# Performance work log

Measured on AMD Instinct MI355X. Metric: run time of the kernel, lower is better.

## Reference

```python
import jax, jax.numpy as jnp
import numpy as np

EPS = 1e-5

def _bn(x, gamma, beta):
    # training-mode BatchNorm1d over (batch, points) per channel; x: [B, C, N]
    mean = x.mean(axis=(0, 2), keepdims=True)
    var = x.var(axis=(0, 2), keepdims=True)
    return gamma[None, :, None] * (x - mean) * jax.lax.rsqrt(var + EPS) + beta[None, :, None]

def _conv_nn(x, idx, W, b):
    # x: [B, Cin, N_in]; idx: [N_out, k]; W: [Cout, Cin, k]
    g = x[:, :, idx]  # gather -> [B, Cin, N_out, k]
    return jnp.einsum('bink,oik->bon', g, W) + b[None, :, None]

def setup_inputs() -> dict:
    key = jax.random.key(0)
    ks = jax.random.split(key, 8)
    B, Cin, Cout = 32, 32, 64
    Nin, Nout, K, KP = 32768, 8192, 9, 4
    s = 0.05
    return {
        'x': jax.random.normal(ks[0], (B, Cin, Nin), jnp.float32),
        'W1': jax.random.normal(ks[1], (Cout, Cin, K), jnp.float32) * s,
        'b1': jnp.zeros((Cout,), jnp.float32),
        'W2': jax.random.normal(ks[2], (Cout, Cout, K), jnp.float32) * s,
        'b2': jnp.zeros((Cout,), jnp.float32),
        'We': jax.random.normal(ks[3], (Cout, Cin), jnp.float32) * s,
        'be': jnp.zeros((Cout,), jnp.float32),
        'g1': jnp.ones((Cout,), jnp.float32), 'beta1': jnp.zeros((Cout,), jnp.float32),
        'g2': jnp.ones((Cout,), jnp.float32), 'beta2': jnp.zeros((Cout,), jnp.float32),
        'g3': jnp.ones((Cout,), jnp.float32), 'beta3': jnp.zeros((Cout,), jnp.float32),
        'idx1': jax.random.randint(ks[4], (Nout, K), 0, Nin, jnp.int32),
        'idx2': jax.random.randint(ks[5], (Nout, K), 0, Nout, jnp.int32),
        'pool_idx': jax.random.randint(ks[6], (Nout, KP), 0, Nin, jnp.int32),
    }

def reference(x, W1, b1, W2, b2, We, be, g1, beta1, g2, beta2, g3, beta3, idx1, idx2, pool_idx):
    # main branch: ConvNN -> BN -> ReLU -> ConvNN -> BN
    out = jax.nn.relu(_bn(_conv_nn(x, idx1, W1, b1), g1, beta1))
    out = _bn(_conv_nn(out, idx2, W2, b2), g2, beta2)
    # shortcut: AvgPoolNN (k=4) -> 1x1 conv expand -> BN
    pooled = x[:, :, pool_idx].mean(axis=-1)  # [B, Cin, N_out]
    identity = _bn(jnp.einsum('bin,oi->bon', pooled, We) + be[None, :, None], g3, beta3)
    return jax.nn.relu(out + identity)
```

## Files before the change

kernel.cpp:

```cpp
#include <hip/hip_runtime.h>
#include <hip/hip_bf16.h>

typedef __attribute__((ext_vector_type(8))) short short8_t;
typedef __attribute__((ext_vector_type(4))) float f32x4_t;

#define NOUT 8192
#define NIN 32768
#define MTOT 262144.0f
#define ST_STRIPES 64

#define MF(a,b,c) __builtin_amdgcn_mfma_f32_16x16x32_bf16((a),(b),(c),0,0,0)

static __device__ __forceinline__ float bf2f(ushort u) {
    union { float f; unsigned int i; } x; x.i = ((unsigned int)u) << 16; return x.f;
}
static __device__ __forceinline__ ushort f2bfx(float f) {
    union { __hip_bfloat16 h; ushort u; } v;
    v.h = __float2bfloat16(f);
    return v.u;
}
static __device__ __forceinline__ short8_t i4s8(int4 v) {
    union { int4 i; short8_t s; } u; u.i = v; return u.s;
}

static __device__ __forceinline__ short8_t bn8(int4 v, const float* a8, const float* c8) {
    ushort* pv = (ushort*)&v;
    #pragma unroll
    for (int e = 0; e < 8; ++e)
        pv[e] = f2bfx(fmaxf(a8[e] * bf2f(pv[e]) + c8[e], 0.f));
    return i4s8(v);
}

__global__ __launch_bounds__(256) void transpose_x_kernel(
    const float* __restrict__ x, ushort* __restrict__ xt)
{
    __shared__ ushort T[64][66];
    const int tid = threadIdx.x;
    const int n0 = blockIdx.x * 64, c0 = blockIdx.y * 64;
    const int lane64 = tid & 63, rb = (tid >> 6) * 16;
    #pragma unroll
    for (int r = 0; r < 16; ++r) {
        int c_l = rb + r;
        T[c_l][lane64] = f2bfx(x[(size_t)(c0 + c_l) * NIN + n0 + lane64]);
    }
    __syncthreads();
    #pragma unroll
    for (int r = 0; r < 16; ++r) {
        int n_l = rb + r;
        xt[(size_t)(n0 + n_l) * 1024 + c0 + lane64] = T[lane64][n_l];
    }
}

__global__ __launch_bounds__(256) void prep_w_kernel(
    const float* __restrict__ W1, const float* __restrict__ W2,
    const float* __restrict__ We,
    ushort* __restrict__ w1p, ushort* __restrict__ w2p, ushort* __restrict__ wep,
    float* __restrict__ stz)
{
    int t = blockIdx.x * 256 + threadIdx.x;
    const int N1 = 18432, N2 = 36864, N3 = 2048;
    if (t < 3 * ST_STRIPES * 128) stz[t] = 0.f;
    if (t < N1) {
        int e = t & 7, o = (t >> 3) & 63, seg = t >> 9;
        int fcg = seg & 3, k = seg >> 2;
        int i = fcg * 8 + e;
        w1p[t] = f2bfx(W1[o * 288 + i * 9 + k]);
    } else if (t < N1 + N2) {
        int t2 = t - N1;
        int e = t2 & 7, o = (t2 >> 3) & 63, seg = t2 >> 9;
        int fcg = seg & 3, kk = (seg >> 2) & 1, k = seg >> 3;
        int ci = kk * 32 + fcg * 8 + e;
        w2p[t2] = f2bfx(W2[o * 576 + ci * 9 + k]);
    } else if (t < N1 + N2 + N3) {
        int t3 = t - N1 - N2;
        wep[t3] = f2bfx(We[t3]);
    }
}

__global__ __launch_bounds__(512, 2) void conv1i_kernel(
    const ushort* __restrict__ xt, const int* __restrict__ idx1,
    const int* __restrict__ pool_idx, const ushort* __restrict__ w1p,
    const ushort* __restrict__ wep,
    ushort* __restrict__ out1, ushort* __restrict__ identt,
    float* __restrict__ st1g, float* __restrict__ st3g)
{
    __shared__ __align__(16) ushort Wl[18432];
    __shared__ float Ls1[128], Ls3[128];
    const int tid = threadIdx.x;
    const int lane = tid & 63, wv = tid >> 6;
    const int n = __builtin_amdgcn_readfirstlane(blockIdx.x * 8 + wv);
    const int l15 = lane & 15, fcg = lane >> 4, fc = fcg * 8;

    for (int i = tid; i < 2304; i += 512)
        ((int4*)Wl)[i] = ((const int4*)w1p)[i];
    if (tid < 128) { Ls1[tid] = 0.f; Ls3[tid] = 0.f; }

    int rows[9], prow[4];
    {
        const int* idxn = idx1 + n * 9;
        #pragma unroll
        for (int t = 0; t < 9; ++t) rows[t] = idxn[t];
        const int* pn = pool_idx + n * 4;
        #pragma unroll
        for (int t = 0; t < 4; ++t) prow[t] = pn[t];
    }
    __syncthreads();

    f32x4_t acc[2][4];
    #pragma unroll
    for (int m = 0; m < 2; ++m)
        #pragma unroll
        for (int nt = 0; nt < 4; ++nt) acc[m][nt] = (f32x4_t){0.f, 0.f, 0.f, 0.f};

    int4 A0[2], A1[2], A2[2], A3[2];

#define C1_PRE(K, A) { \
    const ushort* rp = xt + (size_t)rows[K] * 1024 + l15 * 32 + fc; \
    A[0] = *(const int4*)rp; \
    A[1] = *(const int4*)(rp + 512); }

#define C1_PPRE(KP, A) { \
    const ushort* rp = xt + (size_t)prow[KP] * 1024 + l15 * 32 + fc; \
    A[0] = *(const int4*)rp; \
    A[1] = *(const int4*)(rp + 512); }

#define C1_BODY(K, A) { \
    const ushort* wp = Wl + ((K) * 4 + fcg) * 512; \
    short8_t b0 = *(const short8_t*)(wp + l15 * 8); \
    short8_t b1 = *(const short8_t*)(wp + (16 + l15) * 8); \
    short8_t b2 = *(const short8_t*)(wp + (32 + l15) * 8); \
    short8_t b3 = *(const short8_t*)(wp + (48 + l15) * 8); \
    short8_t af0 = i4s8(A[0]), af1 = i4s8(A[1]); \
    acc[0][0] = MF(af0, b0, acc[0][0]); acc[1][0] = MF(af1, b0, acc[1][0]); \
    acc[0][1] = MF(af0, b1, acc[0][1]); acc[1][1] = MF(af1, b1, acc[1][1]); \
    acc[0][2] = MF(af0, b2, acc[0][2]); acc[1][2] = MF(af1, b2, acc[1][2]); \
    acc[0][3] = MF(af0, b3, acc[0][3]); acc[1][3] = MF(af1, b3, acc[1][3]); }

    C1_PRE(0, A0); C1_PRE(1, A1); C1_PRE(2, A2); C1_PRE(3, A3);
    C1_BODY(0, A0); C1_PRE(4, A0);
    C1_BODY(1, A1); C1_PRE(5, A1);
    C1_BODY(2, A2); C1_PRE(6, A2);
    C1_BODY(3, A3); C1_PRE(7, A3);
    C1_BODY(4, A0); C1_PRE(8, A0);
    C1_BODY(5, A1); C1_PPRE(0, A1);
    C1_BODY(6, A2); C1_PPRE(1, A2);
    C1_BODY(7, A3); C1_PPRE(2, A3);
    C1_BODY(8, A0);
#undef C1_PRE
#undef C1_BODY

    const size_t outbase = (size_t)n * 2048;
    #pragma unroll
    for (int m = 0; m < 2; ++m)
        #pragma unroll
        for (int nt = 0; nt < 4; ++nt)
            #pragma unroll
            for (int j = 0; j < 4; ++j) {
                int b = m * 16 + (lane >> 4) * 4 + j;
                int o = nt * 16 + l15;
                out1[outbase + b * 64 + o] = f2bfx(acc[m][nt][j]);
            }
    #pragma unroll
    for (int nt = 0; nt < 4; ++nt) {
        float s = 0.f, q = 0.f;
        #pragma unroll
        for (int m = 0; m < 2; ++m)
            #pragma unroll
            for (int j = 0; j < 4; ++j) { float v = acc[m][nt][j]; s += v; q += v * v; }
        s += __shfl_xor(s, 16); s += __shfl_xor(s, 32);
        q += __shfl_xor(q, 16); q += __shfl_xor(q, 32);
        if (lane < 16) {
            atomicAdd(&Ls1[nt * 16 + lane], s);
            atomicAdd(&Ls1[64 + nt * 16 + lane], q);
        }
    }

    int4 P3[2];
    C1_PPRE(3, P3);
#undef C1_PPRE
    float s0[8], s1[8];
    #pragma unroll
    for (int e = 0; e < 8; ++e) { s0[e] = 0.f; s1[e] = 0.f; }
    {
        const ushort* p;
        p = (const ushort*)&A1[0];
        #pragma unroll
        for (int e = 0; e < 8; ++e) s0[e] += bf2f(p[e]);
        p = (const ushort*)&A1[1];
        #pragma unroll
        for (int e = 0; e < 8; ++e) s1[e] += bf2f(p[e]);
        p = (const ushort*)&A2[0];
        #pragma unroll
        for (int e = 0; e < 8; ++e) s0[e] += bf2f(p[e]);
        p = (const ushort*)&A2[1];
        #pragma unroll
        for (int e = 0; e < 8; ++e) s1[e] += bf2f(p[e]);
        p = (const ushort*)&A3[0];
        #pragma unroll
        for (int e = 0; e < 8; ++e) s0[e] += bf2f(p[e]);
        p = (const ushort*)&A3[1];
        #pragma unroll
        for (int e = 0; e < 8; ++e) s1[e] += bf2f(p[e]);
        p = (const ushort*)&P3[0];
        #pragma unroll
        for (int e = 0; e < 8; ++e) s0[e] += bf2f(p[e]);
        p = (const ushort*)&P3[1];
        #pragma unroll
        for (int e = 0; e < 8; ++e) s1[e] += bf2f(p[e]);
    }
    short8_t paf0, paf1;
    {
        int4 v0, v1; ushort* p0 = (ushort*)&v0; ushort* p1 = (ushort*)&v1;
        #pragma unroll
        for (int e = 0; e < 8; ++e) {
            p0[e] = f2bfx(s0[e] * 0.25f);
            p1[e] = f2bfx(s1[e] * 0.25f);
        }
        paf0 = i4s8(v0); paf1 = i4s8(v1);
    }
    short8_t bfr[4];
    {
        const ushort* wpf = wep + l15 * 32 + fc;
        #pragma unroll
        for (int nt = 0; nt < 4; ++nt)
            bfr[nt] = *(const short8_t*)(wpf + nt * 512);
    }
    #pragma unroll
    for (int nt = 0; nt < 4; ++nt) {
        acc[0][nt] = (f32x4_t){0.f, 0.f, 0.f, 0.f};
        acc[1][nt] = (f32x4_t){0.f, 0.f, 0.f, 0.f};
        acc[0][nt] = MF(paf0, bfr[nt], acc[0][nt]);
        acc[1][nt] = MF(paf1, bfr[nt], acc[1][nt]);
    }
    #pragma unroll
    for (int m = 0; m < 2; ++m)
        #pragma unroll
        for (int nt = 0; nt < 4; ++nt)
            #pragma unroll
            for (int j = 0; j < 4; ++j) {
                int b = m * 16 + (lane >> 4) * 4 + j;
                int o = nt * 16 + l15;
                identt[outbase + b * 64 + o] = f2bfx(acc[m][nt][j]);
            }
    #pragma unroll
    for (int nt = 0; nt < 4; ++nt) {
        float s = 0.f, q = 0.f;
        #pragma unroll
        for (int m = 0; m < 2; ++m)
            #pragma unroll
            for (int j = 0; j < 4; ++j) { float v = acc[m][nt][j]; s += v; q += v * v; }
        s += __shfl_xor(s, 16); s += __shfl_xor(s, 32);
        q += __shfl_xor(q, 16); q += __shfl_xor(q, 32);
        if (lane < 16) {
            atomicAdd(&Ls3[nt * 16 + lane], s);
            atomicAdd(&Ls3[64 + nt * 16 + lane], q);
        }
    }
    __syncthreads();
    if (tid < 128) {
        atomicAdd(&st1g[(blockIdx.x & (ST_STRIPES - 1)) * 128 + tid], Ls1[tid]);
        atomicAdd(&st3g[(blockIdx.x & (ST_STRIPES - 1)) * 128 + tid], Ls3[tid]);
    }
}

__global__ __launch_bounds__(512, 2) void conv2_kernel(
    const ushort* __restrict__ out1raw, const int* __restrict__ idx2,
    const ushort* __restrict__ w2p, const float* __restrict__ ac1,
    ushort* __restrict__ out2, float* __restrict__ st)
{
    __shared__ __align__(16) ushort Wl[36864];
    __shared__ float Ls[128];
    const int tid = threadIdx.x;
    const int lane = tid & 63, wv = tid >> 6;
    const int n = __builtin_amdgcn_readfirstlane(blockIdx.x * 8 + wv);
    const int l15 = lane & 15, fcg = lane >> 4, fc = fcg * 8;

    for (int i = tid; i < 4608; i += 512)
        ((int4*)Wl)[i] = ((const int4*)w2p)[i];
    if (tid < 128) Ls[tid] = 0.f;

    int rows[9];
    {
        const int* idxn = idx2 + n * 9;
        #pragma unroll
        for (int t = 0; t < 9; ++t) rows[t] = idxn[t];
    }
    float a0r[8], c0r[8], a1r[8], c1r[8];
    #pragma unroll
    for (int e = 0; e < 8; ++e) {
        a0r[e] = ac1[fc + e];       c0r[e] = ac1[64 + fc + e];
        a1r[e] = ac1[32 + fc + e];  c1r[e] = ac1[96 + fc + e];
    }
    __syncthreads();

    f32x4_t acc[2][4];
    #pragma unroll
    for (int m = 0; m < 2; ++m)
        #pragma unroll
        for (int nt = 0; nt < 4; ++nt) acc[m][nt] = (f32x4_t){0.f, 0.f, 0.f, 0.f};

    int4 A0[4], A1[4], A2[4];

#define C2_PRE(K, A) { \
    const ushort* rp = out1raw + (size_t)rows[K] * 2048 + l15 * 64 + fc; \
    A[0] = *(const int4*)rp; \
    A[1] = *(const int4*)(rp + 32); \
    A[2] = *(const int4*)(rp + 1024); \
    A[3] = *(const int4*)(rp + 1056); }

#define C2_BODY(K, A) { \
    const ushort* wp0 = Wl + ((K) * 8 + fcg) * 512; \
    const ushort* wp1 = wp0 + 4 * 512; \
    short8_t b00 = *(const short8_t*)(wp0 + l15 * 8); \
    short8_t b10 = *(const short8_t*)(wp0 + (16 + l15) * 8); \
    short8_t b20 = *(const short8_t*)(wp0 + (32 + l15) * 8); \
    short8_t b30 = *(const short8_t*)(wp0 + (48 + l15) * 8); \
    short8_t b01 = *(const short8_t*)(wp1 + l15 * 8); \
    short8_t b11 = *(const short8_t*)(wp1 + (16 + l15) * 8); \
    short8_t b21 = *(const short8_t*)(wp1 + (32 + l15) * 8); \
    short8_t b31 = *(const short8_t*)(wp1 + (48 + l15) * 8); \
    short8_t af00 = bn8(A[0], a0r, c0r); \
    short8_t af01 = bn8(A[1], a1r, c1r); \
    short8_t af10 = bn8(A[2], a0r, c0r); \
    short8_t af11 = bn8(A[3], a1r, c1r); \
    acc[0][0] = MF(af00, b00, acc[0][0]); acc[0][0] = MF(af01, b01, acc[0][0]); \
    acc[0][1] = MF(af00, b10, acc[0][1]); acc[0][1] = MF(af01, b11, acc[0][1]); \
    acc[0][2] = MF(af00, b20, acc[0][2]); acc[0][2] = MF(af01, b21, acc[0][2]); \
    acc[0][3] = MF(af00, b30, acc[0][3]); acc[0][3] = MF(af01, b31, acc[0][3]); \
    acc[1][0] = MF(af10, b00, acc[1][0]); acc[1][0] = MF(af11, b01, acc[1][0]); \
    acc[1][1] = MF(af10, b10, acc[1][1]); acc[1][1] = MF(af11, b11, acc[1][1]); \
    acc[1][2] = MF(af10, b20, acc[1][2]); acc[1][2] = MF(af11, b21, acc[1][2]); \
    acc[1][3] = MF(af10, b30, acc[1][3]); acc[1][3] = MF(af11, b31, acc[1][3]); }

    C2_PRE(0, A0); C2_PRE(1, A1); C2_PRE(2, A2);
    C2_BODY(0, A0); C2_PRE(3, A0);
    C2_BODY(1, A1); C2_PRE(4, A1);
    C2_BODY(2, A2); C2_PRE(5, A2);
    C2_BODY(3, A0); C2_PRE(6, A0);
    C2_BODY(4, A1); C2_PRE(7, A1);
    C2_BODY(5, A2); C2_PRE(8, A2);
    C2_BODY(6, A0);
    C2_BODY(7, A1);
    C2_BODY(8, A2);
#undef C2_PRE
#undef C2_BODY

    const size_t outbase = (size_t)n * 2048;
    #pragma unroll
    for (int m = 0; m < 2; ++m)
        #pragma unroll
        for (int nt = 0; nt < 4; ++nt)
            #pragma unroll
            for (int j = 0; j < 4; ++j) {
                int b = m * 16 + (lane >> 4) * 4 + j;
                int o = nt * 16 + l15;
                out2[outbase + b * 64 + o] = f2bfx(acc[m][nt][j]);
            }
    #pragma unroll
    for (int nt = 0; nt < 4; ++nt) {
        float s = 0.f, q = 0.f;
        #pragma unroll
        for (int m = 0; m < 2; ++m)
            #pragma unroll
            for (int j = 0; j < 4; ++j) { float v = acc[m][nt][j]; s += v; q += v * v; }
        s += __shfl_xor(s, 16); s += __shfl_xor(s, 32);
        q += __shfl_xor(q, 16); q += __shfl_xor(q, 32);
        if (lane < 16) {
            atomicAdd(&Ls[nt * 16 + lane], s);
            atomicAdd(&Ls[64 + nt * 16 + lane], q);
        }
    }
    __syncthreads();
    if (tid < 128) atomicAdd(&st[(blockIdx.x & (ST_STRIPES - 1)) * 128 + tid], Ls[tid]);
}

__global__ void finalize_kernel(const float* __restrict__ st, const float* __restrict__ g,
                                const float* __restrict__ bet, float* __restrict__ ac)
{
    int o = threadIdx.x;
    if (o >= 64) return;
    float s = 0.f, q = 0.f;
    for (int i = 0; i < ST_STRIPES; ++i) { s += st[i * 128 + o]; q += st[i * 128 + 64 + o]; }
    float mean = s * (1.0f / MTOT);
    float var  = q * (1.0f / MTOT) - mean * mean;
    float a = g[o] * rsqrtf(var + 1e-5f);
    ac[o] = a;
    ac[64 + o] = bet[o] - a * mean;
}

__global__ void finalize_dual_kernel(
    const float* __restrict__ stA, const float* __restrict__ gA, const float* __restrict__ bA,
    const float* __restrict__ stB, const float* __restrict__ gB, const float* __restrict__ bB,
    float* __restrict__ acA, float* __restrict__ acB)
{
    int o = threadIdx.x;
    if (o >= 64) return;
    const float* st = blockIdx.x ? stB : stA;
    const float* g  = blockIdx.x ? gB  : gA;
    const float* bt = blockIdx.x ? bB  : bA;
    float* ac       = blockIdx.x ? acB : acA;
    float s = 0.f, q = 0.f;
    for (int i = 0; i < ST_STRIPES; ++i) { s += st[i * 128 + o]; q += st[i * 128 + 64 + o]; }
    float mean = s * (1.0f / MTOT);
    float var  = q * (1.0f / MTOT) - mean * mean;
    float a = g[o] * rsqrtf(var + 1e-5f);
    ac[o] = a;
    ac[64 + o] = bt[o] - a * mean;
}

__global__ __launch_bounds__(256) void final_combine_kernel(
    const ushort* __restrict__ out2, const ushort* __restrict__ idt,
    const float* __restrict__ ac2, const float* __restrict__ ac3,
    float* __restrict__ dout)
{
    __shared__ float tile[64][65];
    const int tid = threadIdx.x;
    const int n0 = blockIdx.x * 64, bo0 = blockIdx.y * 64;
    const int lane64 = tid & 63, rb = (tid >> 6) * 16;
    const int o = lane64;
    const float a2 = ac2[o], c2 = ac2[64 + o], a3 = ac3[o], c3 = ac3[64 + o];
    #pragma unroll
    for (int r = 0; r < 16; ++r) {
        int n_l = rb + r;
        size_t p = (size_t)(n0 + n_l) * 2048 + bo0 + lane64;
        float v = a2 * bf2f(out2[p]) + c2 + a3 * bf2f(idt[p]) + c3;
        tile[n_l][lane64] = fmaxf(v, 0.f);
    }
    __syncthreads();
    #pragma unroll
    for (int r = 0; r < 16; ++r) {
        int bo_l = rb + r;
        dout[(size_t)(bo0 + bo_l) * NOUT + n0 + lane64] = tile[lane64][bo_l];
    }
}

extern "C" void kernel_launch(void* const* d_in, const int* in_sizes, int n_in,
                              void* d_out, int out_size, void* d_ws, size_t ws_size,
                              hipStream_t stream)
{
    const float* x     = (const float*)d_in[0];
    const float* W1    = (const float*)d_in[1];
    const float* W2    = (const float*)d_in[3];
    const float* We    = (const float*)d_in[5];
    const float* g1    = (const float*)d_in[7];
    const float* beta1 = (const float*)d_in[8];
    const float* g2    = (const float*)d_in[9];
    const float* beta2 = (const float*)d_in[10];
    const float* g3    = (const float*)d_in[11];
    const float* beta3 = (const float*)d_in[12];
    const int* idx1    = (const int*)d_in[13];
    const int* idx2    = (const int*)d_in[14];
    const int* pool_idx= (const int*)d_in[15];
    float* dout = (float*)d_out;

    char* ws = (char*)d_ws;
    const size_t off_xt   = 0;
    const size_t off_out1 = 67108864;
    const size_t off_out2 = 100663296;
    const size_t off_id   = 134217728;
    const size_t off_w1p  = 167772160;
    const size_t off_w2p  = 167809024;
    const size_t off_wep  = 167882752;
    const size_t off_st   = 167886848;
    const size_t off_ac   = 167985152;
    const size_t need     = 167986688;
    if (ws_size < need) return;

    ushort* xt   = (ushort*)(ws + off_xt);
    ushort* out1 = (ushort*)(ws + off_out1);
    ushort* out2 = (ushort*)(ws + off_out2);
    ushort* idt  = (ushort*)(ws + off_id);
    ushort* w1p  = (ushort*)(ws + off_w1p);
    ushort* w2p  = (ushort*)(ws + off_w2p);
    ushort* wep  = (ushort*)(ws + off_wep);
    float*  st1  = (float*)(ws + off_st);
    float*  st2  = st1 + 64 * 128;
    float*  st3  = st1 + 2 * 64 * 128;
    float*  ac1  = (float*)(ws + off_ac);
    float*  ac2  = ac1 + 128;
    float*  ac3  = ac1 + 256;

    prep_w_kernel<<<224, 256, 0, stream>>>(W1, W2, We, w1p, w2p, wep, st1);
    transpose_x_kernel<<<dim3(512, 16), 256, 0, stream>>>(x, xt);
    conv1i_kernel<<<1024, 512, 0, stream>>>(xt, idx1, pool_idx, w1p, wep, out1, idt, st1, st3);
    finalize_dual_kernel<<<2, 64, 0, stream>>>(st1, g1, beta1, st3, g3, beta3, ac1, ac3);
    conv2_kernel<<<1024, 512, 0, stream>>>(out1, idx2, w2p, ac1, out2, st2);
    finalize_kernel<<<1, 64, 0, stream>>>(st2, g2, beta2, ac2);
    final_combine_kernel<<<dim3(128, 32), 256, 0, stream>>>(out2, idt, ac2, ac3, dout);
}
```

Measured before the change: 174.4 us.

## Stream gathered rows into LDS via async global_load_lds double buffering

```diff
diff --git a/kernel.cpp b/kernel.cpp
--- a/kernel.cpp
+++ b/kernel.cpp
@@ -10,6 +10,8 @@
 #define ST_STRIPES 64
 
 #define MF(a,b,c) __builtin_amdgcn_mfma_f32_16x16x32_bf16((a),(b),(c),0,0,0)
+#define SB() __builtin_amdgcn_sched_barrier(0)
+#define VW(N) asm volatile("s_waitcnt vmcnt(" #N ")" ::: "memory")
 
 static __device__ __forceinline__ float bf2f(ushort u) {
     union { float f; unsigned int i; } x; x.i = ((unsigned int)u) << 16; return x.f;
@@ -22,6 +24,11 @@
 static __device__ __forceinline__ short8_t i4s8(int4 v) {
     union { int4 i; short8_t s; } u; u.i = v; return u.s;
 }
+static __device__ __forceinline__ void gll16(const ushort* g, ushort* l) {
+    __builtin_amdgcn_global_load_lds(
+        (const __attribute__((address_space(1))) void*)(g),
+        (__attribute__((address_space(3))) void*)(l), 16, 0, 0);
+}
 
 static __device__ __forceinline__ short8_t bn8(int4 v, const float* a8, const float* c8) {
     ushort* pv = (ushort*)&v;
@@ -36,18 +43,20 @@
 {
     __shared__ ushort T[64][66];
     const int tid = threadIdx.x;
-    const int n0 = blockIdx.x * 64, c0 = blockIdx.y * 64;
+    const int n0 = blockIdx.x * 64;
+    const int b0 = (blockIdx.y >> 2) * 8, g = blockIdx.y & 3;
     const int lane64 = tid & 63, rb = (tid >> 6) * 16;
     #pragma unroll
     for (int r = 0; r < 16; ++r) {
         int c_l = rb + r;
-        T[c_l][lane64] = f2bfx(x[(size_t)(c0 + c_l) * NIN + n0 + lane64]);
+        int row = (b0 + (c_l >> 3)) * 32 + g * 8 + (c_l & 7);
+        T[c_l][lane64] = f2bfx(x[(size_t)row * NIN + n0 + lane64]);
     }
     __syncthreads();
     #pragma unroll
     for (int r = 0; r < 16; ++r) {
         int n_l = rb + r;
-        xt[(size_t)(n0 + n_l) * 1024 + c0 + lane64] = T[lane64][n_l];
+        xt[(size_t)(n0 + n_l) * 1024 + g * 256 + b0 * 8 + lane64] = T[lane64][n_l];
     }
 }
 
@@ -85,11 +94,14 @@
     float* __restrict__ st1g, float* __restrict__ st3g)
 {
     __shared__ __align__(16) ushort Wl[18432];
+    __shared__ __align__(16) ushort Ar[16384];
     __shared__ float Ls1[128], Ls3[128];
     const int tid = threadIdx.x;
     const int lane = tid & 63, wv = tid >> 6;
     const int n = __builtin_amdgcn_readfirstlane(blockIdx.x * 8 + wv);
     const int l15 = lane & 15, fcg = lane >> 4, fc = fcg * 8;
+    ushort* S0 = Ar + wv * 2048;
+    ushort* S1 = S0 + 1024;
 
     for (int i = tid; i < 2304; i += 512)
         ((int4*)Wl)[i] = ((const int4*)w1p)[i];
@@ -112,41 +124,43 @@
         #pragma unroll
         for (int nt = 0; nt < 4; ++nt) acc[m][nt] = (f32x4_t){0.f, 0.f, 0.f, 0.f};
 
-    int4 A0[2], A1[2], A2[2], A3[2];
-
-#define C1_PRE(K, A) { \
-    const ushort* rp = xt + (size_t)rows[K] * 1024 + l15 * 32 + fc; \
-    A[0] = *(const int4*)rp; \
-    A[1] = *(const int4*)(rp + 512); }
-
-#define C1_PPRE(KP, A) { \
-    const ushort* rp = xt + (size_t)prow[KP] * 1024 + l15 * 32 + fc; \
-    A[0] = *(const int4*)rp; \
-    A[1] = *(const int4*)(rp + 512); }
-
-#define C1_BODY(K, A) { \
+#define C1_ISSUE(K, S) { \
+    const ushort* src = xt + (size_t)rows[K] * 1024 + lane * 8; \
+    gll16(src, (S)); \
+    gll16(src + 512, (S) + 512); }
+
+#define C1_BODY(K, S) { \
     const ushort* wp = Wl + ((K) * 4 + fcg) * 512; \
     short8_t b0 = *(const short8_t*)(wp + l15 * 8); \
     short8_t b1 = *(const short8_t*)(wp + (16 + l15) * 8); \
     short8_t b2 = *(const short8_t*)(wp + (32 + l15) * 8); \
     short8_t b3 = *(const short8_t*)(wp + (48 + l15) * 8); \
-    short8_t af0 = i4s8(A[0]), af1 = i4s8(A[1]); \
+    short8_t af0 = *(const short8_t*)((S) + fcg * 256 + l15 * 8); \
+    short8_t af1 = *(const short8_t*)((S) + fcg * 256 + 128 + l15 * 8); \
     acc[0][0] = MF(af0, b0, acc[0][0]); acc[1][0] = MF(af1, b0, acc[1][0]); \
     acc[0][1] = MF(af0, b1, acc[0][1]); acc[1][1] = MF(af1, b1, acc[1][1]); \
     acc[0][2] = MF(af0, b2, acc[0][2]); acc[1][2] = MF(af1, b2, acc[1][2]); \
     acc[0][3] = MF(af0, b3, acc[0][3]); acc[1][3] = MF(af1, b3, acc[1][3]); }
 
-    C1_PRE(0, A0); C1_PRE(1, A1); C1_PRE(2, A2); C1_PRE(3, A3);
-    C1_BODY(0, A0); C1_PRE(4, A0);
-    C1_BODY(1, A1); C1_PRE(5, A1);
-    C1_BODY(2, A2); C1_PRE(6, A2);
-    C1_BODY(3, A3); C1_PRE(7, A3);
-    C1_BODY(4, A0); C1_PRE(8, A0);
-    C1_BODY(5, A1); C1_PPRE(0, A1);
-    C1_BODY(6, A2); C1_PPRE(1, A2);
-    C1_BODY(7, A3); C1_PPRE(2, A3);
-    C1_BODY(8, A0);
-#undef C1_PRE
+    C1_ISSUE(0, S0); C1_ISSUE(1, S1); SB();
+    VW(2); SB(); C1_BODY(0, S0); SB(); C1_ISSUE(2, S0); SB();
+    VW(2); SB(); C1_BODY(1, S1); SB(); C1_ISSUE(3, S1); SB();
+    VW(2); SB(); C1_BODY(2, S0); SB(); C1_ISSUE(4, S0); SB();
+    VW(2); SB(); C1_BODY(3, S1); SB(); C1_ISSUE(5, S1); SB();
+    VW(2); SB(); C1_BODY(4, S0); SB(); C1_ISSUE(6, S0); SB();
+    VW(2); SB(); C1_BODY(5, S1); SB(); C1_ISSUE(7, S1); SB();
+    VW(2); SB(); C1_BODY(6, S0); SB(); C1_ISSUE(8, S0); SB();
+    VW(2); SB(); C1_BODY(7, S1); SB();
+    int4 Pa0, Pa1, Pb0, Pb1, Pc0, Pc1, Pd0, Pd1;
+#define C1_PLOAD(KP, X, Y) { \
+    const ushort* rp = xt + (size_t)prow[KP] * 1024 + fcg * 256 + l15 * 8; \
+    X = *(const int4*)rp; Y = *(const int4*)(rp + 128); }
+    C1_PLOAD(0, Pa0, Pa1); C1_PLOAD(1, Pb0, Pb1);
+    C1_PLOAD(2, Pc0, Pc1); C1_PLOAD(3, Pd0, Pd1);
+#undef C1_PLOAD
+    SB();
+    VW(8); SB(); C1_BODY(8, S0);
+#undef C1_ISSUE
 #undef C1_BODY
 
     const size_t outbase = (size_t)n * 2048;
@@ -158,7 +172,7 @@
             for (int j = 0; j < 4; ++j) {
                 int b = m * 16 + (lane >> 4) * 4 + j;
                 int o = nt * 16 + l15;
-                out1[outbase + b * 64 + o] = f2bfx(acc[m][nt][j]);
+                out1[outbase + (o >> 3) * 256 + b * 8 + (o & 7)] = f2bfx(acc[m][nt][j]);
             }
     #pragma unroll
     for (int nt = 0; nt < 4; ++nt) {
@@ -175,36 +189,34 @@
         }
     }
 
-    int4 P3[2];
-    C1_PPRE(3, P3);
-#undef C1_PPRE
     float s0[8], s1[8];
     #pragma unroll
     for (int e = 0; e < 8; ++e) { s0[e] = 0.f; s1[e] = 0.f; }
     {
         const ushort* p;
-        p = (const ushort*)&A1[0];
+        p = (const ushort*)&Pa0; \
+        
         #pragma unroll
         for (int e = 0; e < 8; ++e) s0[e] += bf2f(p[e]);
-        p = (const ushort*)&A1[1];
+        p = (const ushort*)&Pa1;
         #pragma unroll
         for (int e = 0; e < 8; ++e) s1[e] += bf2f(p[e]);
-        p = (const ushort*)&A2[0];
+        p = (const ushort*)&Pb0;
         #pragma unroll
         for (int e = 0; e < 8; ++e) s0[e] += bf2f(p[e]);
-        p = (const ushort*)&A2[1];
+        p = (const ushort*)&Pb1;
         #pragma unroll
         for (int e = 0; e < 8; ++e) s1[e] += bf2f(p[e]);
-        p = (const ushort*)&A3[0];
+        p = (const ushort*)&Pc0;
         #pragma unroll
         for (int e = 0; e < 8; ++e) s0[e] += bf2f(p[e]);
-        p = (const ushort*)&A3[1];
+        p = (const ushort*)&Pc1;
         #pragma unroll
         for (int e = 0; e < 8; ++e) s1[e] += bf2f(p[e]);
-        p = (const ushort*)&P3[0];
+        p = (const ushort*)&Pd0;
         #pragma unroll
         for (int e = 0; e < 8; ++e) s0[e] += bf2f(p[e]);
-        p = (const ushort*)&P3[1];
+        p = (const ushort*)&Pd1;
         #pragma unroll
         for (int e = 0; e < 8; ++e) s1[e] += bf2f(p[e]);
     }
@@ -269,11 +281,14 @@
     ushort* __restrict__ out2, float* __restrict__ st)
 {
     __shared__ __align__(16) ushort Wl[36864];
+    __shared__ __align__(16) ushort Ar[32768];
     __shared__ float Ls[128];
     const int tid = threadIdx.x;
     const int lane = tid & 63, wv = tid >> 6;
     const int n = __builtin_amdgcn_readfirstlane(blockIdx.x * 8 + wv);
     const int l15 = lane & 15, fcg = lane >> 4, fc = fcg * 8;
+    ushort* S0 = Ar + wv * 4096;
+    ushort* S1 = S0 + 2048;
 
     for (int i = tid; i < 4608; i += 512)
         ((int4*)Wl)[i] = ((const int4*)w2p)[i];
@@ -299,18 +314,16 @@
         #pragma unroll
         for (int nt = 0; nt < 4; ++nt) acc[m][nt] = (f32x4_t){0.f, 0.f, 0.f, 0.f};
 
-    int4 A0[4], A1[4], A2[4];
-
-#define C2_PRE(K, A) { \
-    const ushort* rp = out1raw + (size_t)rows[K] * 2048 + l15 * 64 + fc; \
-    A[0] = *(const int4*)rp; \
-    A[1] = *(const int4*)(rp + 32); \
-    A[2] = *(const int4*)(rp + 1024); \
-    A[3] = *(const int4*)(rp + 1056); }
-
-#define C2_BODY(K, A) { \
+#define C2_ISSUE(K, S) { \
+    const ushort* src = out1raw + (size_t)rows[K] * 2048 + lane * 8; \
+    gll16(src, (S)); \
+    gll16(src + 512, (S) + 512); \
+    gll16(src + 1024, (S) + 1024); \
+    gll16(src + 1536, (S) + 1536); }
+
+#define C2_BODY(K, S) { \
     const ushort* wp0 = Wl + ((K) * 8 + fcg) * 512; \
-    const ushort* wp1 = wp0 + 4 * 512; \
+    const ushort* wp1 = wp0 + 2048; \
     short8_t b00 = *(const short8_t*)(wp0 + l15 * 8); \
     short8_t b10 = *(const short8_t*)(wp0 + (16 + l15) * 8); \
     short8_t b20 = *(const short8_t*)(wp0 + (32 + l15) * 8); \
@@ -319,10 +332,14 @@
     short8_t b11 = *(const short8_t*)(wp1 + (16 + l15) * 8); \
     short8_t b21 = *(const short8_t*)(wp1 + (32 + l15) * 8); \
     short8_t b31 = *(const short8_t*)(wp1 + (48 + l15) * 8); \
-    short8_t af00 = bn8(A[0], a0r, c0r); \
-    short8_t af01 = bn8(A[1], a1r, c1r); \
-    short8_t af10 = bn8(A[2], a0r, c0r); \
-    short8_t af11 = bn8(A[3], a1r, c1r); \
+    int4 q00 = *(const int4*)((S) + fcg * 256 + l15 * 8); \
+    int4 q01 = *(const int4*)((S) + 1024 + fcg * 256 + l15 * 8); \
+    int4 q10 = *(const int4*)((S) + fcg * 256 + 128 + l15 * 8); \
+    int4 q11 = *(const int4*)((S) + 1024 + fcg * 256 + 128 + l15 * 8); \
+    short8_t af00 = bn8(q00, a0r, c0r); \
+    short8_t af01 = bn8(q01, a1r, c1r); \
+    short8_t af10 = bn8(q10, a0r, c0r); \
+    short8_t af11 = bn8(q11, a1r, c1r); \
     acc[0][0] = MF(af00, b00, acc[0][0]); acc[0][0] = MF(af01, b01, acc[0][0]); \
     acc[0][1] = MF(af00, b10, acc[0][1]); acc[0][1] = MF(af01, b11, acc[0][1]); \
     acc[0][2] = MF(af00, b20, acc[0][2]); acc[0][2] = MF(af01, b21, acc[0][2]); \
@@ -332,17 +349,17 @@
     acc[1][2] = MF(af10, b20, acc[1][2]); acc[1][2] = MF(af11, b21, acc[1][2]); \
     acc[1][3] = MF(af10, b30, acc[1][3]); acc[1][3] = MF(af11, b31, acc[1][3]); }
 
-    C2_PRE(0, A0); C2_PRE(1, A1); C2_PRE(2, A2);
-    C2_BODY(0, A0); C2_PRE(3, A0);
-    C2_BODY(1, A1); C2_PRE(4, A1);
-    C2_BODY(2, A2); C2_PRE(5, A2);
-    C2_BODY(3, A0); C2_PRE(6, A0);
-    C2_BODY(4, A1); C2_PRE(7, A1);
-    C2_BODY(5, A2); C2_PRE(8, A2);
-    C2_BODY(6, A0);
-    C2_BODY(7, A1);
-    C2_BODY(8, A2);
-#undef C2_PRE
+    C2_ISSUE(0, S0); C2_ISSUE(1, S1); SB();
+    VW(4); SB(); C2_BODY(0, S0); SB(); C2_ISSUE(2, S0); SB();
+    VW(4); SB(); C2_BODY(1, S1); SB(); C2_ISSUE(3, S1); SB();
+    VW(4); SB(); C2_BODY(2, S0); SB(); C2_ISSUE(4, S0); SB();
+    VW(4); SB(); C2_BODY(3, S1); SB(); C2_ISSUE(5, S1); SB();
+    VW(4); SB(); C2_BODY(4, S0); SB(); C2_ISSUE(6, S0); SB();
+    VW(4); SB(); C2_BODY(5, S1); SB(); C2_ISSUE(7, S1); SB();
+    VW(4); SB(); C2_BODY(6, S0); SB(); C2_ISSUE(8, S0); SB();
+    VW(4); SB(); C2_BODY(7, S1); SB();
+    VW(0); SB(); C2_BODY(8, S0);
+#undef C2_ISSUE
 #undef C2_BODY
 
     const size_t outbase = (size_t)n * 2048;
```

Measured after the change: 192.4 us. 10.3% more time.
